# Kernel optimization log

Hardware: AMD Instinct MI355X
Metric: run time of the kernel (lower is better)

## Reference

```python
import jax, jax.numpy as jnp
import numpy as np

OUT_K = 7  # out_kernel


def setup_inputs() -> dict:
    key = jax.random.key(0)
    k = jax.random.split(key, 12)
    b, cin, h, w = 2, 256, 64, 64
    C, pd = 64, 4          # out_channels, pos_dim
    qc = C - pd            # channels produced by conv_q/k/v
    s = 0.05
    f32 = jnp.float32
    return {
        "x":    jax.random.normal(k[0], (b, cin, h, w), f32),
        "Wq":   jax.random.normal(k[1], (qc, cin), f32) * s,
        "bq":   jax.random.normal(k[2], (qc,), f32) * s,
        "Wk":   jax.random.normal(k[3], (qc, cin), f32) * s,
        "bk":   jax.random.normal(k[4], (qc,), f32) * s,
        "Wv":   jax.random.normal(k[5], (qc, cin), f32) * s,
        "bv":   jax.random.normal(k[6], (qc,), f32) * s,
        "Wp":   jax.random.normal(k[7], (pd, 2), f32) * s,
        "bp":   jax.random.normal(k[8], (pd,), f32) * s,
        "Wout": jax.random.normal(k[9], (C, C, OUT_K, OUT_K), f32) * s,
        "bout": jax.random.normal(k[10], (C,), f32) * s,
    }


def reference(x, Wq, bq, Wk, bk, Wv, bv, Wp, bp, Wout, bout):
    b, cin, h, w = x.shape
    C = Wout.shape[0]  # out_channels
    dt = x.dtype

    # positional encoding: hw_pose is (row_index, col_index) grids -> 1x1 conv to pos_dim chans
    rows = jnp.broadcast_to(jnp.arange(h, dtype=dt)[:, None], (h, w))
    cols = jnp.broadcast_to(jnp.arange(w, dtype=dt)[None, :], (h, w))
    grid = jnp.stack([rows, cols], axis=0)                      # (2,h,w)
    pos = jnp.einsum('oc,chw->ohw', Wp, grid) + bp[:, None, None]  # (pd,h,w)
    pos = jnp.broadcast_to(pos[None], (b,) + pos.shape)         # (b,pd,h,w)

    def conv1x1(W, bias):
        return jnp.einsum('bchw,oc->bohw', x, W) + bias[None, :, None, None]

    qs = jnp.concatenate([conv1x1(Wq, bq), pos], axis=1)        # (b,C,h,w)
    ks = jnp.concatenate([conv1x1(Wk, bk), pos], axis=1)
    vs = jnp.concatenate([conv1x1(Wv, bv), pos], axis=1)

    hw = h * w
    qsf = qs.transpose(0, 2, 3, 1).reshape(b, hw, C)            # (b,hw,C)
    ksf = ks.reshape(b, C, hw)                                  # (b,C,hw)
    vsf = vs.transpose(0, 2, 3, 1)                              # (b,h,w,C)

    qk = jnp.einsum('bnc,bcm->bnm', qsf, ksf) / jnp.sqrt(jnp.asarray(C, dt))
    diag = jnp.arange(hw)
    qk = qk.at[:, diag, diag].set(0.0)                          # zero diagonal BEFORE softmax
    attn = jax.nn.softmax(qk, axis=-1).reshape(b, h, w, h, w)

    # 7x7 clamped neighborhood gather (replaces the 49-iteration python loop)
    r = OUT_K // 2
    offs = jnp.arange(-r, r + 1)
    hi = jnp.clip(jnp.arange(h)[:, None] + offs[None, :], 0, h - 1)  # (h,7)
    wi = jnp.clip(jnp.arange(w)[:, None] + offs[None, :], 0, w - 1)  # (w,7)
    ii = jnp.arange(h)[:, None, None, None]
    jj = jnp.arange(w)[None, :, None, None]
    hk = hi[:, None, :, None]
    wk = wi[None, :, None, :]
    attn_loc = attn[:, ii, jj, hk, wk]                          # (b,h,w,7,7)
    v_loc = vsf[:, hk, wk, :]                                   # (b,h,w,7,7,C)

    qkv = attn_loc[..., None] * v_loc                           # (b,h,w,7,7,C)
    # con_out: kernel=7, stride=7 over a 7x7 patch == full contraction
    out = jnp.einsum('bhwklc,ockl->bhwo', qkv, Wout) + bout     # (b,h,w,C)
    out = jax.nn.relu(out)
    return out.transpose(0, 3, 1, 2)                            # (b,C,h,w)
```

## Files before the change

### kernel.cpp

```cpp
#include <hip/hip_runtime.h>
#include <math.h>

#define NTAP 49

typedef short bf16x8 __attribute__((ext_vector_type(8)));
typedef float f32x4  __attribute__((ext_vector_type(4)));

__device__ __forceinline__ float b2f(ushort u) {
    return __uint_as_float(((unsigned)u) << 16);
}
__device__ __forceinline__ ushort f2b(float f) {
    unsigned u = __float_as_uint(f);
    return (ushort)((u + 0x7FFFu + ((u >> 16) & 1u)) >> 16);
}
__device__ __forceinline__ int iclamp(int x) { return min(max(x, 0), 63); }

#define LOG2E 1.44269504f
#define S2    (0.125f * LOG2E)

#define WTB_OFF 0u
#define QH_OFF  598016u
#define KH_OFF  1646592u
#define VH_OFF  2695168u
#define LP_OFF  3743744u
#define MXQ_OFF 4005888u
#define MXK_OFF 4006912u

__device__ __forceinline__ float mh_reduce(const float* __restrict__ MXq,
                                           const float* __restrict__ MXk,
                                           int b, int t, float* sh) {
    if (t < 64) {
        float a = fmaxf(MXq[(b << 7) + t], MXq[(b << 7) + 64 + t]);
        float k = fmaxf(MXk[(b << 7) + t], MXk[(b << 7) + 64 + t]);
        #pragma unroll
        for (int off = 1; off < 64; off <<= 1) {
            a = fmaxf(a, __shfl_xor(a, off, 64));
            k = fmaxf(k, __shfl_xor(k, off, 64));
        }
        if (t == 0) *sh = 0.125f * sqrtf(a) * sqrtf(k) + 1.0f;
    }
    __syncthreads();
    return *sh;
}

__global__ __launch_bounds__(512, 2) void k_qkv(
    const float* __restrict__ x,
    const float* __restrict__ Wq, const float* __restrict__ Wk, const float* __restrict__ Wv,
    const float* __restrict__ bq, const float* __restrict__ bk, const float* __restrict__ bv,
    const float* __restrict__ Wp, const float* __restrict__ bp,
    ushort* __restrict__ QKV, float* __restrict__ MXq, float* __restrict__ MXk)
{
    __shared__ ushort Xh[32 * 256];
    __shared__ ushort Xl[32 * 256];
    __shared__ ushort Wshl[192 * 64];
    __shared__ float  sqL[64];
    int bid = blockIdx.x;
    int b   = bid >> 7;
    int n0  = (bid & 127) * 32;
    int t   = threadIdx.x;
    int w    = t >> 6;
    int L    = t & 63;
    int lrow = L & 15, lk = L >> 4;

    if (t < 64) sqL[t] = 0.f;
    {
        int p  = t & 31;
        int cg = t >> 5;
        #pragma unroll
        for (int it = 0; it < 2; ++it) {
            int cgi = cg + it * 16;
            float v[8];
            #pragma unroll
            for (int e = 0; e < 8; ++e)
                v[e] = x[((size_t)(b * 256 + cgi * 8 + e) << 12) + n0 + p];
            bf16x8 hi, lo;
            #pragma unroll
            for (int e = 0; e < 8; ++e) {
                ushort h = f2b(v[e]);
                hi[e] = (short)h;
                lo[e] = (short)f2b(v[e] - b2f(h));
            }
            int off = p * 256 + ((cgi * 8) ^ ((p & 7) * 8));
            *(bf16x8*)(Xh + off) = hi;
            *(bf16x8*)(Xl + off) = lo;
        }
    }

    int   s_och[3], s_g[3];
    bool  s_live[3];
    const float* s_src[3];
    #pragma unroll
    for (int s = 0; s < 3; ++s) {
        int g_idx = t + s * 512;
        int och = g_idx >> 3, g = g_idx & 7;
        int mat = och >> 6, o = och & 63;
        const float* Wm = (mat == 0) ? Wq : (mat == 1) ? Wk : Wv;
        s_och[s] = och; s_g[s] = g;
        s_live[s] = (o < 60);
        s_src[s] = Wm + o * 256 + (g & 3) * 8;
    }
    float4 wreg[3][2];

    #define ISSUE_W(c8) {                                                   \
        _Pragma("unroll")                                                   \
        for (int s = 0; s < 3; ++s) {                                       \
            if (s_live[s]) {                                                \
                const float* sp = s_src[s] + (c8) * 32;                     \
                wreg[s][0] = *(const float4*)(sp);                          \
                wreg[s][1] = *(const float4*)(sp + 4);                      \
            } else {                                                        \
                wreg[s][0] = make_float4(0.f,0.f,0.f,0.f);                  \
                wreg[s][1] = make_float4(0.f,0.f,0.f,0.f);                  \
            }                                                               \
        } }
    #define WRITE_W() {                                                     \
        _Pragma("unroll")                                                   \
        for (int s = 0; s < 3; ++s) {                                       \
            float vv[8] = {wreg[s][0].x, wreg[s][0].y, wreg[s][0].z,        \
                           wreg[s][0].w, wreg[s][1].x, wreg[s][1].y,        \
                           wreg[s][1].z, wreg[s][1].w};                     \
            bf16x8 val;                                                     \
            _Pragma("unroll")                                               \
            for (int e = 0; e < 8; ++e) {                                   \
                ushort h = f2b(vv[e]);                                      \
                val[e] = (s_g[s] < 4) ? (short)h                            \
                                      : (short)f2b(vv[e] - b2f(h));         \
            }                                                               \
            *(bf16x8*)((char*)Wshl + s_och[s] * 128 +                       \
                       ((s_g[s] * 16) ^ ((s_och[s] & 7) << 4))) = val;      \
        } }

    ISSUE_W(0);
    __syncthreads();
    WRITE_W();
    __syncthreads();

    int pxh = w >> 2;
    int ob  = (w & 3) * 48;
    int px  = pxh * 16 + lrow;

    f32x4 acc[3] = {{0,0,0,0},{0,0,0,0},{0,0,0,0}};

    for (int c8 = 0; c8 < 8; ++c8) {
        if (c8 + 1 < 8) ISSUE_W(c8 + 1);
        int cidx = (c8 * 4 + lk) * 8;
        int o0 = px * 256 + (cidx ^ ((px & 7) * 8));
        bf16x8 ah = *(const bf16x8*)(Xh + o0);
        bf16x8 al = *(const bf16x8*)(Xl + o0);
        #pragma unroll
        for (int c = 0; c < 3; ++c) {
            int och = ob + c * 16 + lrow;
            const char* wb = (const char*)Wshl + och * 128;
            int swz = (och & 7) << 4;
            bf16x8 bh = *(const bf16x8*)(wb + ((lk * 16) ^ swz));
            bf16x8 bl = *(const bf16x8*)(wb + (((4 + lk) * 16) ^ swz));
            acc[c] = __builtin_amdgcn_mfma_f32_16x16x32_bf16(al, bh, acc[c], 0, 0, 0);
            acc[c] = __builtin_amdgcn_mfma_f32_16x16x32_bf16(ah, bl, acc[c], 0, 0, 0);
            acc[c] = __builtin_amdgcn_mfma_f32_16x16x32_bf16(ah, bh, acc[c], 0, 0, 0);
        }
        __syncthreads();
        if (c8 + 1 < 8) WRITE_W();
        __syncthreads();
    }

    float s_q[4] = {0,0,0,0}, s_k[4] = {0,0,0,0};
    #pragma unroll
    for (int c = 0; c < 3; ++c) {
        int och = ob + c * 16 + lrow;
        int mat = och >> 6;
        int o   = och & 63;
        const float* bm = (mat == 0) ? bq : (mat == 1) ? bk : bv;
        ushort* Ob = QKV + (size_t)mat * 524288;
        if (o < 60) {
            float bias = bm[o];
            #pragma unroll
            for (int e = 0; e < 4; ++e) {
                int n = n0 + pxh * 16 + lk * 4 + e;
                float v = acc[c][e] + bias;
                Ob[((size_t)((b << 12) + n)) * 64 + o] = f2b(v);
                if (mat == 0) s_q[e] = fmaf(v, v, s_q[e]);
                else if (mat == 1) s_k[e] = fmaf(v, v, s_k[e]);
            }
        } else {
            int po = o - 60;
            float w0 = Wp[2 * po], w1 = Wp[2 * po + 1], b0 = bp[po];
            #pragma unroll
            for (int e = 0; e < 4; ++e) {
                int n = n0 + pxh * 16 + lk * 4 + e;
                float fi = (float)(n >> 6), fj = (float)(n & 63);
                float pv = fmaf(w0, fi, fmaf(w1, fj, b0));
                Ob[((size_t)((b << 12) + n)) * 64 + o] = f2b(pv);
                if (mat == 0) s_q[e] = fmaf(pv, pv, s_q[e]);
                else if (mat == 1) s_k[e] = fmaf(pv, pv, s_k[e]);
            }
        }
    }
    #pragma unroll
    for (int off = 1; off < 16; off <<= 1) {
        #pragma unroll
        for (int e = 0; e < 4; ++e) {
            s_q[e] += __shfl_xor(s_q[e], off, 64);
            s_k[e] += __shfl_xor(s_k[e], off, 64);
        }
    }
    if (lrow == 0) {
        #pragma unroll
        for (int e = 0; e < 4; ++e) {
            int pix = pxh * 16 + lk * 4 + e;
            atomicAdd(&sqL[pix],      s_q[e]);
            atomicAdd(&sqL[32 + pix], s_k[e]);
        }
    }
    __syncthreads();
    if (t < 32) {
        float q2 = sqL[t], k2 = sqL[32 + t];
        #pragma unroll
        for (int off = 1; off < 32; off <<= 1) {
            q2 = fmaxf(q2, __shfl_xor(q2, off, 64));
            k2 = fmaxf(k2, __shfl_xor(k2, off, 64));
        }
        if (t == 0) { MXq[bid] = q2; MXk[bid] = k2; }
    }
}

__global__ __launch_bounds__(512, 2) void k_stats(
    const float* __restrict__ Wout, ushort* __restrict__ Wtb,
    const ushort* __restrict__ QH, const ushort* __restrict__ KH,
    const float* __restrict__ MXq, const float* __restrict__ MXk,
    float* __restrict__ Lp)
{
    __shared__ ushort Ks[2][128 * 64];
    __shared__ float  mhs;
    int bid = blockIdx.x;
    int ks  = bid & 7;
    int r   = bid >> 3;
    int b   = r >> 5;
    int n0  = (r & 31) * 128;
    int ck0 = ks * 512;
    int t = threadIdx.x;

    {
        int widx = bid * 512 + t;
        if (widx < 64 * 64 * NTAP) {
            int o   = widx / (64 * NTAP);
            int rem = widx - o * (64 * NTAP);
            int c   = rem / NTAP;
            int kl  = rem - c * NTAP;
            Wtb[(o * NTAP + kl) * 64 + c] = f2b(Wout[widx]);
        }
    }
    float bse = -mh_reduce(MXq, MXk, b, t, &mhs) * LOG2E;

    int w = t >> 6, L = t & 63;
    int lrow = L & 15, lk = L >> 4;

    size_t qbase = ((size_t)((b << 12) + n0 + w * 16 + lrow)) * 64 + lk * 8;
    bf16x8 a0 = *(const bf16x8*)(QH + qbase);
    bf16x8 a1 = *(const bf16x8*)(QH + qbase + 32);

    #pragma unroll
    for (int gi = 0; gi < 2; ++gi) {
        int g = t + gi * 512;
        int u = g >> 3, c8 = g & 7;
        bf16x8 val = *(const bf16x8*)(KH + ((size_t)((b << 12) + ck0 + u)) * 64 + c8 * 8);
        *(bf16x8*)((char*)Ks[0] + u * 128 + ((c8 * 16) ^ ((u & 7) << 4))) = val;
    }

    float rs0 = 0.f, rs1 = 0.f, rs2 = 0.f, rs3 = 0.f;

    for (int c = 0; c < 4; ++c) {
        bf16x8 st0, st1;
        int u0 = t >> 3, c80 = t & 7;
        int u1 = (t + 512) >> 3, c81 = t & 7;
        bool pf = (c + 1) < 4;
        if (pf) {
            st0 = *(const bf16x8*)(KH + ((size_t)((b << 12) + ck0 + (c + 1) * 128 + u0)) * 64 + c80 * 8);
            st1 = *(const bf16x8*)(KH + ((size_t)((b << 12) + ck0 + (c + 1) * 128 + u1)) * 64 + c81 * 8);
        }
        __syncthreads();
        const char* kb = (const char*)Ks[c & 1];
        #pragma unroll
        for (int kg = 0; kg < 8; ++kg) {
            int u = kg * 16 + lrow;
            int swz = (u & 7) << 4;
            bf16x8 b0 = *(const bf16x8*)(kb + u * 128 + ((lk * 16) ^ swz));
            bf16x8 b1 = *(const bf16x8*)(kb + u * 128 + ((64 + lk * 16) ^ swz));
            f32x4 z = {0.f, 0.f, 0.f, 0.f};
            z = __builtin_amdgcn_mfma_f32_16x16x32_bf16(a0, b0, z, 0, 0, 0);
            z = __builtin_amdgcn_mfma_f32_16x16x32_bf16(a1, b1, z, 0, 0, 0);
            rs0 += exp2f(fmaf(z[0], S2, bse));
            rs1 += exp2f(fmaf(z[1], S2, bse));
            rs2 += exp2f(fmaf(z[2], S2, bse));
            rs3 += exp2f(fmaf(z[3], S2, bse));
        }
        if (pf) {
            char* kn = (char*)Ks[(c + 1) & 1];
            *(bf16x8*)(kn + u0 * 128 + ((c80 * 16) ^ ((u0 & 7) << 4))) = st0;
            *(bf16x8*)(kn + u1 * 128 + ((c81 * 16) ^ ((u1 & 7) << 4))) = st1;
        }
    }
    #pragma unroll
    for (int off = 1; off < 16; off <<= 1) {
        rs0 += __shfl_xor(rs0, off, 64);
        rs1 += __shfl_xor(rs1, off, 64);
        rs2 += __shfl_xor(rs2, off, 64);
        rs3 += __shfl_xor(rs3, off, 64);
    }
    if (lrow == 0) {
        float* dst = Lp + ((size_t)(ks * 2 + b) << 12) + n0 + w * 16 + lk * 4;
        dst[0] = rs0; dst[1] = rs1; dst[2] = rs2; dst[3] = rs3;
    }
}

__global__ __launch_bounds__(512, 2) void k_out(
    const ushort* __restrict__ QH, const ushort* __restrict__ KH,
    const ushort* __restrict__ VH, const ushort* __restrict__ Wtb,
    const float* __restrict__ Lp,
    const float* __restrict__ MXq, const float* __restrict__ MXk,
    const float* __restrict__ bout, float* __restrict__ out)
{
    __shared__ ushort Vs[7 * 40 * 64];
    __shared__ ushort Kh[7 * 40 * 64];
    __shared__ ushort Ws[7 * 64 * 64];
    __shared__ float  Al2[NTAP * 36];
    __shared__ float  Lrow[32];
    __shared__ float  LcS[32];
    __shared__ float  mhs;
    int bid = blockIdx.x;
    int b   = bid >> 7;
    int rem = bid & 127;
    int i   = rem >> 1;
    int j0  = (rem & 1) * 32;
    int n0  = (i << 6) + j0;
    int t   = threadIdx.x;
    int w    = t >> 6;
    int L    = t & 63;
    int lrow = L & 15, lk = L >> 4;

    float bse = -mh_reduce(MXq, MXk, b, t, &mhs) * LOG2E;
    float e0  = exp2f(bse);

    bf16x8 wreg[7];
    #define ISSUE_WS(kk) {                                                          \
        _Pragma("unroll")                                                           \
        for (int s = 0; s < 7; ++s) {                                               \
            int g = t + s * 512;                                                    \
            int c8 = g & 7, och = (g >> 3) & 63, ll = g >> 9;                       \
            wreg[s] = *(const bf16x8*)(Wtb + ((size_t)(och * NTAP + (kk) * 7 + ll)) * 64 + c8 * 8); \
        } }
    #define WRITE_WS() {                                                            \
        _Pragma("unroll")                                                           \
        for (int s = 0; s < 7; ++s) {                                               \
            int g = t + s * 512;                                                    \
            int c8 = g & 7, och = (g >> 3) & 63, ll = g >> 9;                       \
            *(bf16x8*)((char*)Ws + ll * 8192 + och * 128 +                          \
                       ((c8 * 16) ^ ((och & 7) << 4))) = wreg[s];                   \
        } }

    for (int g = t; g < 2 * 7 * 38 * 8; g += 512) {
        int which = g >= 7 * 38 * 8;
        int gg = which ? g - 7 * 38 * 8 : g;
        int kk = gg / 304;
        int r2 = gg - kk * 304;
        int u  = r2 >> 3, c8 = r2 & 7;
        int vr = iclamp(i + kk - 3);
        int vc = iclamp(j0 - 3 + u);
        const ushort* src = which ? KH : VH;
        ushort* dst = which ? Kh : Vs;
        bf16x8 val = *(const bf16x8*)(src + ((size_t)((b << 12) + (vr << 6) + vc)) * 64 + c8 * 8);
        *(bf16x8*)((char*)dst + kk * 5120 + u * 128 + ((c8 * 16) ^ ((u & 7) << 4))) = val;
    }
    ISSUE_WS(0);
    WRITE_WS();
    if (t < 32) {
        int n = n0 + t;
        float s = 0.f;
        #pragma unroll
        for (int ks = 0; ks < 8; ++ks)
            s += Lp[((size_t)(ks * 2 + b) << 12) + n];
        Lrow[t] = s;
    }
    __syncthreads();

    {
        int p = t >> 4, u = t & 15;
        int n = n0 + p;
        int pj = n & 63;
        const ushort* qr = QH + ((size_t)(b << 12) + n) * 64;
        bf16x8 qv[8];
        #pragma unroll
        for (int c8 = 0; c8 < 8; ++c8) qv[c8] = *(const bf16x8*)(qr + c8 * 8);

        int nt = (u == 0) ? 4 : 3;
        float d[4] = {0.f, 0.f, 0.f, 0.f};
        int srcs[4];
        const char* kbp[4];
        int swzs[4];
        #pragma unroll
        for (int m = 0; m < 4; ++m) {
            int tap = (m == 3) ? 48 : (u + 16 * m);
            int kk = tap / 7, ll = tap - kk * 7;
            srcs[m] = (iclamp(i + kk - 3) << 6) + iclamp(pj + ll - 3);
            int uu = p + ll;
            kbp[m]  = (const char*)Kh + kk * 5120 + uu * 128;
            swzs[m] = (uu & 7) << 4;
        }
        #pragma unroll
        for (int c8 = 0; c8 < 8; ++c8) {
            bf16x8 kv0 = *(const bf16x8*)(kbp[0] + ((c8 * 16) ^ swzs[0]));
            bf16x8 kv1 = *(const bf16x8*)(kbp[1] + ((c8 * 16) ^ swzs[1]));
            bf16x8 kv2 = *(const bf16x8*)(kbp[2] + ((c8 * 16) ^ swzs[2]));
            #pragma unroll
            for (int e = 0; e < 8; ++e) {
                float q = b2f((ushort)qv[c8][e]);
                d[0] = fmaf(q, b2f((ushort)kv0[e]), d[0]);
                d[1] = fmaf(q, b2f((ushort)kv1[e]), d[1]);
                d[2] = fmaf(q, b2f((ushort)kv2[e]), d[2]);
            }
        }
        if (nt == 4) {
            #pragma unroll
            for (int c8 = 0; c8 < 8; ++c8) {
                bf16x8 kv3 = *(const bf16x8*)(kbp[3] + ((c8 * 16) ^ swzs[3]));
                #pragma unroll
                for (int e = 0; e < 8; ++e)
                    d[3] = fmaf(b2f((ushort)qv[c8][e]), b2f((ushort)kv3[e]), d[3]);
            }
        }
        if (u == 8)
            LcS[p] = Lrow[p] - exp2f(fmaf(d[1], S2, bse)) + e0;
        __syncthreads();
        float rLc = 1.0f / LcS[p];
        for (int m = 0; m < nt; ++m) {
            int tap = (m == 3) ? 48 : (u + 16 * m);
            float A = (srcs[m] == n) ? (e0 * rLc)
                                     : (exp2f(fmaf(d[m], S2, bse)) * rLc);
            Al2[tap * 36 + p] = A;
        }
    }
    __syncthreads();

    int q16 = (w >> 2) << 4;
    int o16 = (w & 3) << 4;
    int oA  = o16 + lrow;
    int wswz = (oA & 7) << 4;
    f32x4 acc0 = {0.f, 0.f, 0.f, 0.f};

    for (int kk = 0; kk < 7; ++kk) {
        if (kk + 1 < 7) ISSUE_WS(kk + 1);
        const char* vrow = (const char*)Vs + kk * 5120;
        #pragma unroll
        for (int ll = 0; ll < 7; ++ll) {
            int kl = kk * 7 + ll;
            int u = q16 + lrow + ll;
            const char* vb = vrow + u * 128;
            int swz = (u & 7) << 4;
            bf16x8 v0 = *(const bf16x8*)(vb + ((lk * 16) ^ swz));
            bf16x8 v1 = *(const bf16x8*)(vb + ((64 + lk * 16) ^ swz));
            float4 av = *(const float4*)(&Al2[kl * 36 + q16 + lk * 4]);
            const char* wb = (const char*)Ws + ll * 8192 + oA * 128;
            bf16x8 b00 = *(const bf16x8*)(wb + ((lk * 16) ^ wswz));
            bf16x8 b01 = *(const bf16x8*)(wb + (((4 + lk) * 16) ^ wswz));
            f32x4 z = {0.f, 0.f, 0.f, 0.f};
            z = __builtin_amdgcn_mfma_f32_16x16x32_bf16(v0, b00, z, 0, 0, 0);
            z = __builtin_amdgcn_mfma_f32_16x16x32_bf16(v1, b01, z, 0, 0, 0);
            acc0[0] = fmaf(av.x, z[0], acc0[0]);
            acc0[1] = fmaf(av.y, z[1], acc0[1]);
            acc0[2] = fmaf(av.z, z[2], acc0[2]);
            acc0[3] = fmaf(av.w, z[3], acc0[3]);
        }
        __syncthreads();
        if (kk + 1 < 7) WRITE_WS();
        __syncthreads();
    }

    int o = oA;
    int nbase = n0 + q16 + lk * 4;
    float bb = bout[o];
    float4 v = make_float4(fmaxf(acc0[0] + bb, 0.f), fmaxf(acc0[1] + bb, 0.f),
                           fmaxf(acc0[2] + bb, 0.f), fmaxf(acc0[3] + bb, 0.f));
    *(float4*)(out + (((size_t)(b * 64 + o)) << 12) + nbase) = v;
}

extern "C" void kernel_launch(void* const* d_in, const int* in_sizes, int n_in,
                              void* d_out, int out_size, void* d_ws, size_t ws_size,
                              hipStream_t stream) {
    const float* x    = (const float*)d_in[0];
    const float* Wq   = (const float*)d_in[1];
    const float* bq   = (const float*)d_in[2];
    const float* Wk   = (const float*)d_in[3];
    const float* bk   = (const float*)d_in[4];
    const float* Wv   = (const float*)d_in[5];
    const float* bv   = (const float*)d_in[6];
    const float* Wp   = (const float*)d_in[7];
    const float* bp   = (const float*)d_in[8];
    const float* Wout = (const float*)d_in[9];
    const float* bout = (const float*)d_in[10];
    float* out = (float*)d_out;

    char* ws = (char*)d_ws;
    ushort* Wtb = (ushort*)(ws + WTB_OFF);
    ushort* QKV = (ushort*)(ws + QH_OFF);
    float*  Lp  = (float*)(ws + LP_OFF);
    float*  MXq = (float*)(ws + MXQ_OFF);
    float*  MXk = (float*)(ws + MXK_OFF);

    ushort* QH = QKV;
    ushort* KH = QKV + 524288;
    ushort* VH = QKV + 1048576;

    hipLaunchKernelGGL(k_qkv,   dim3(256), dim3(512), 0, stream,
                       x, Wq, Wk, Wv, bq, bk, bv, Wp, bp, QKV, MXq, MXk);
    hipLaunchKernelGGL(k_stats, dim3(512), dim3(512), 0, stream,
                       Wout, Wtb, QH, KH, MXq, MXk, Lp);
    hipLaunchKernelGGL(k_out,   dim3(256), dim3(512), 0, stream,
                       QH, KH, VH, Wtb, Lp, MXq, MXk, bout, out);
}
```

Baseline: 50.54 us.

## Split warps by tap in k_out and double rows per warp in row-sum kernel

The row-sum kernel now has each warp cover 32 query rows over half the key chunk, reusing each K fragment for two MFMA pairs. This doubles the number of partial-sum planes, and the LSE reader in k_out is widened to match. In k_out, warps are assigned one horizontal tap each (7 active of 8) and compute all 32x64 outputs, so W fragments are reused across two query tiles. A shared-memory cross-warp reduction then sums the per-warp results. Shared memory grows to about 136KB, which drops occupancy to one block per CU, and one warp sits idle in the main loop.

Result: slower. 54.09 us (+7.0%).

```diff
diff --git a/kernel.cpp b/kernel.cpp
--- a/kernel.cpp
+++ b/kernel.cpp
@@ -23,8 +23,8 @@
 #define KH_OFF  1646592u
 #define VH_OFF  2695168u
 #define LP_OFF  3743744u
-#define MXQ_OFF 4005888u
-#define MXK_OFF 4006912u
+#define MXQ_OFF 4268032u
+#define MXK_OFF 4269056u
 
 __device__ __forceinline__ float mh_reduce(const float* __restrict__ MXq,
                                            const float* __restrict__ MXk,
@@ -253,10 +253,14 @@
 
     int w = t >> 6, L = t & 63;
     int lrow = L & 15, lk = L >> 4;
-
-    size_t qbase = ((size_t)((b << 12) + n0 + w * 16 + lrow)) * 64 + lk * 8;
-    bf16x8 a0 = *(const bf16x8*)(QH + qbase);
-    bf16x8 a1 = *(const bf16x8*)(QH + qbase + 32);
+    int rg = w & 3, kh = w >> 2;
+    int rbase = n0 + rg * 32;
+
+    size_t qb = ((size_t)((b << 12) + rbase + lrow)) * 64 + lk * 8;
+    bf16x8 a0 = *(const bf16x8*)(QH + qb);
+    bf16x8 a1 = *(const bf16x8*)(QH + qb + 32);
+    bf16x8 a2 = *(const bf16x8*)(QH + qb + 1024);
+    bf16x8 a3 = *(const bf16x8*)(QH + qb + 1024 + 32);
 
     #pragma unroll
     for (int gi = 0; gi < 2; ++gi) {
@@ -266,7 +270,7 @@
         *(bf16x8*)((char*)Ks[0] + u * 128 + ((c8 * 16) ^ ((u & 7) << 4))) = val;
     }
 
-    float rs0 = 0.f, rs1 = 0.f, rs2 = 0.f, rs3 = 0.f;
+    float rs0=0,rs1=0,rs2=0,rs3=0,rs4=0,rs5=0,rs6=0,rs7=0;
 
     for (int c = 0; c < 4; ++c) {
         bf16x8 st0, st1;
@@ -280,18 +284,24 @@
         __syncthreads();
         const char* kb = (const char*)Ks[c & 1];
         #pragma unroll
-        for (int kg = 0; kg < 8; ++kg) {
-            int u = kg * 16 + lrow;
+        for (int kg = 0; kg < 4; ++kg) {
+            int u = kh * 64 + kg * 16 + lrow;
             int swz = (u & 7) << 4;
             bf16x8 b0 = *(const bf16x8*)(kb + u * 128 + ((lk * 16) ^ swz));
             bf16x8 b1 = *(const bf16x8*)(kb + u * 128 + ((64 + lk * 16) ^ swz));
-            f32x4 z = {0.f, 0.f, 0.f, 0.f};
-            z = __builtin_amdgcn_mfma_f32_16x16x32_bf16(a0, b0, z, 0, 0, 0);
-            z = __builtin_amdgcn_mfma_f32_16x16x32_bf16(a1, b1, z, 0, 0, 0);
-            rs0 += exp2f(fmaf(z[0], S2, bse));
-            rs1 += exp2f(fmaf(z[1], S2, bse));
-            rs2 += exp2f(fmaf(z[2], S2, bse));
-            rs3 += exp2f(fmaf(z[3], S2, bse));
+            f32x4 z0 = {0,0,0,0}, z1 = {0,0,0,0};
+            z0 = __builtin_amdgcn_mfma_f32_16x16x32_bf16(a0, b0, z0, 0, 0, 0);
+            z0 = __builtin_amdgcn_mfma_f32_16x16x32_bf16(a1, b1, z0, 0, 0, 0);
+            z1 = __builtin_amdgcn_mfma_f32_16x16x32_bf16(a2, b0, z1, 0, 0, 0);
+            z1 = __builtin_amdgcn_mfma_f32_16x16x32_bf16(a3, b1, z1, 0, 0, 0);
+            rs0 += exp2f(fmaf(z0[0], S2, bse));
+            rs1 += exp2f(fmaf(z0[1], S2, bse));
+            rs2 += exp2f(fmaf(z0[2], S2, bse));
+            rs3 += exp2f(fmaf(z0[3], S2, bse));
+            rs4 += exp2f(fmaf(z1[0], S2, bse));
+            rs5 += exp2f(fmaf(z1[1], S2, bse));
+            rs6 += exp2f(fmaf(z1[2], S2, bse));
+            rs7 += exp2f(fmaf(z1[3], S2, bse));
         }
         if (pf) {
             char* kn = (char*)Ks[(c + 1) & 1];
@@ -301,31 +311,41 @@
     }
     #pragma unroll
     for (int off = 1; off < 16; off <<= 1) {
-        rs0 += __shfl_xor(rs0, off, 64);
-        rs1 += __shfl_xor(rs1, off, 64);
-        rs2 += __shfl_xor(rs2, off, 64);
-        rs3 += __shfl_xor(rs3, off, 64);
+        rs0 += __shfl_xor(rs0, off, 64); rs1 += __shfl_xor(rs1, off, 64);
+        rs2 += __shfl_xor(rs2, off, 64); rs3 += __shfl_xor(rs3, off, 64);
+        rs4 += __shfl_xor(rs4, off, 64); rs5 += __shfl_xor(rs5, off, 64);
+        rs6 += __shfl_xor(rs6, off, 64); rs7 += __shfl_xor(rs7, off, 64);
     }
     if (lrow == 0) {
-        float* dst = Lp + ((size_t)(ks * 2 + b) << 12) + n0 + w * 16 + lk * 4;
+        int plane = ks * 2 + kh;
+        float* dst = Lp + ((size_t)(plane * 2 + b) << 12) + rbase + lk * 4;
         dst[0] = rs0; dst[1] = rs1; dst[2] = rs2; dst[3] = rs3;
-    }
-}
-
-__global__ __launch_bounds__(512, 2) void k_out(
+        dst[16] = rs4; dst[17] = rs5; dst[18] = rs6; dst[19] = rs7;
+    }
+}
+
+#define SM_VS   0
+#define SM_KH   35840
+#define SM_WS   71680
+#define SM_AL2  129024
+#define SM_LROW 136080
+#define SM_LCS  136208
+#define SM_MHS  136336
+__global__ __launch_bounds__(512, 1) void k_out(
     const ushort* __restrict__ QH, const ushort* __restrict__ KH,
     const ushort* __restrict__ VH, const ushort* __restrict__ Wtb,
     const float* __restrict__ Lp,
     const float* __restrict__ MXq, const float* __restrict__ MXk,
     const float* __restrict__ bout, float* __restrict__ out)
 {
-    __shared__ ushort Vs[7 * 40 * 64];
-    __shared__ ushort Kh[7 * 40 * 64];
-    __shared__ ushort Ws[7 * 64 * 64];
-    __shared__ float  Al2[NTAP * 36];
-    __shared__ float  Lrow[32];
-    __shared__ float  LcS[32];
-    __shared__ float  mhs;
+    __shared__ __align__(16) char smem[136448];
+    char*  Vsb  = smem + SM_VS;
+    char*  Khb  = smem + SM_KH;
+    char*  Wsb  = smem + SM_WS;
+    float* Al2  = (float*)(smem + SM_AL2);
+    float* Lrow = (float*)(smem + SM_LROW);
+    float* LcS  = (float*)(smem + SM_LCS);
+
     int bid = blockIdx.x;
     int b   = bid >> 7;
     int rem = bid & 127;
@@ -337,7 +357,7 @@
     int L    = t & 63;
     int lrow = L & 15, lk = L >> 4;
 
-    float bse = -mh_reduce(MXq, MXk, b, t, &mhs) * LOG2E;
+    float bse = -mh_reduce(MXq, MXk, b, t, (float*)(smem + SM_MHS)) * LOG2E;
     float e0  = exp2f(bse);
 
     bf16x8 wreg[7];
@@ -345,15 +365,15 @@
         _Pragma("unroll")                                                           \
         for (int s = 0; s < 7; ++s) {                                               \
             int g = t + s * 512;                                                    \
-            int c8 = g & 7, och = (g >> 3) & 63, ll = g >> 9;                       \
-            wreg[s] = *(const bf16x8*)(Wtb + ((size_t)(och * NTAP + (kk) * 7 + ll)) * 64 + c8 * 8); \
+            int c8 = g & 7, och = (g >> 3) & 63, ll2 = g >> 9;                      \
+            wreg[s] = *(const bf16x8*)(Wtb + ((size_t)(och * NTAP + (kk) * 7 + ll2)) * 64 + c8 * 8); \
         } }
     #define WRITE_WS() {                                                            \
         _Pragma("unroll")                                                           \
         for (int s = 0; s < 7; ++s) {                                               \
             int g = t + s * 512;                                                    \
-            int c8 = g & 7, och = (g >> 3) & 63, ll = g >> 9;                       \
-            *(bf16x8*)((char*)Ws + ll * 8192 + och * 128 +                          \
+            int c8 = g & 7, och = (g >> 3) & 63, ll2 = g >> 9;                      \
+            *(bf16x8*)(Wsb + ll2 * 8192 + och * 128 +                               \
                        ((c8 * 16) ^ ((och & 7) << 4))) = wreg[s];                   \
         } }
 
@@ -366,9 +386,9 @@
         int vr = iclamp(i + kk - 3);
         int vc = iclamp(j0 - 3 + u);
         const ushort* src = which ? KH : VH;
-        ushort* dst = which ? Kh : Vs;
+        char* dst = which ? Khb : Vsb;
         bf16x8 val = *(const bf16x8*)(src + ((size_t)((b << 12) + (vr << 6) + vc)) * 64 + c8 * 8);
-        *(bf16x8*)((char*)dst + kk * 5120 + u * 128 + ((c8 * 16) ^ ((u & 7) << 4))) = val;
+        *(bf16x8*)(dst + kk * 5120 + u * 128 + ((c8 * 16) ^ ((u & 7) << 4))) = val;
     }
     ISSUE_WS(0);
     WRITE_WS();
@@ -376,8 +396,8 @@
         int n = n0 + t;
         float s = 0.f;
         #pragma unroll
-        for (int ks = 0; ks < 8; ++ks)
-            s += Lp[((size_t)(ks * 2 + b) << 12) + n];
+        for (int p = 0; p < 16; ++p)
+            s += Lp[((size_t)(p * 2 + b) << 12) + n];
         Lrow[t] = s;
     }
     __syncthreads();
@@ -402,7 +422,7 @@
             int kk = tap / 7, ll = tap - kk * 7;
             srcs[m] = (iclamp(i + kk - 3) << 6) + iclamp(pj + ll - 3);
             int uu = p + ll;
-            kbp[m]  = (const char*)Kh + kk * 5120 + uu * 128;
+            kbp[m]  = Khb + kk * 5120 + uu * 128;
             swzs[m] = (uu & 7) << 4;
         }
         #pragma unroll
@@ -440,46 +460,73 @@
     }
     __syncthreads();
 
-    int q16 = (w >> 2) << 4;
-    int o16 = (w & 3) << 4;
-    int oA  = o16 + lrow;
-    int wswz = (oA & 7) << 4;
-    f32x4 acc0 = {0.f, 0.f, 0.f, 0.f};
+    int ll = w;
+    bool active = (w < 7);
+    f32x4 acc[2][4] = {{{0,0,0,0},{0,0,0,0},{0,0,0,0},{0,0,0,0}},
+                       {{0,0,0,0},{0,0,0,0},{0,0,0,0},{0,0,0,0}}};
 
     for (int kk = 0; kk < 7; ++kk) {
         if (kk + 1 < 7) ISSUE_WS(kk + 1);
-        const char* vrow = (const char*)Vs + kk * 5120;
-        #pragma unroll
-        for (int ll = 0; ll < 7; ++ll) {
+        if (active) {
             int kl = kk * 7 + ll;
-            int u = q16 + lrow + ll;
-            const char* vb = vrow + u * 128;
-            int swz = (u & 7) << 4;
-            bf16x8 v0 = *(const bf16x8*)(vb + ((lk * 16) ^ swz));
-            bf16x8 v1 = *(const bf16x8*)(vb + ((64 + lk * 16) ^ swz));
-            float4 av = *(const float4*)(&Al2[kl * 36 + q16 + lk * 4]);
-            const char* wb = (const char*)Ws + ll * 8192 + oA * 128;
-            bf16x8 b00 = *(const bf16x8*)(wb + ((lk * 16) ^ wswz));
-            bf16x8 b01 = *(const bf16x8*)(wb + (((4 + lk) * 16) ^ wswz));
-            f32x4 z = {0.f, 0.f, 0.f, 0.f};
-            z = __builtin_amdgcn_mfma_f32_16x16x32_bf16(v0, b00, z, 0, 0, 0);
-            z = __builtin_amdgcn_mfma_f32_16x16x32_bf16(v1, b01, z, 0, 0, 0);
-            acc0[0] = fmaf(av.x, z[0], acc0[0]);
-            acc0[1] = fmaf(av.y, z[1], acc0[1]);
-            acc0[2] = fmaf(av.z, z[2], acc0[2]);
-            acc0[3] = fmaf(av.w, z[3], acc0[3]);
+            const char* vrow = Vsb + kk * 5120;
+            bf16x8 va[2][2];
+            float4 av[2];
+            #pragma unroll
+            for (int qt = 0; qt < 2; ++qt) {
+                int u = qt * 16 + lrow + ll;
+                const char* vb = vrow + u * 128;
+                int swz = (u & 7) << 4;
+                va[qt][0] = *(const bf16x8*)(vb + ((lk * 16) ^ swz));
+                va[qt][1] = *(const bf16x8*)(vb + ((64 + lk * 16) ^ swz));
+                av[qt] = *(const float4*)(Al2 + kl * 36 + qt * 16 + lk * 4);
+            }
+            #pragma unroll
+            for (int ot = 0; ot < 4; ++ot) {
+                int oA = ot * 16 + lrow;
+                const char* wb = Wsb + ll * 8192 + oA * 128;
+                int wswz = (oA & 7) << 4;
+                bf16x8 b00 = *(const bf16x8*)(wb + ((lk * 16) ^ wswz));
+                bf16x8 b01 = *(const bf16x8*)(wb + (((4 + lk) * 16) ^ wswz));
+                #pragma unroll
+                for (int qt = 0; qt < 2; ++qt) {
+                    f32x4 z = {0.f, 0.f, 0.f, 0.f};
+                    z = __builtin_amdgcn_mfma_f32_16x16x32_bf16(va[qt][0], b00, z, 0, 0, 0);
+                    z = __builtin_amdgcn_mfma_f32_16x16x32_bf16(va[qt][1], b01, z, 0, 0, 0);
+                    acc[qt][ot][0] = fmaf(av[qt].x, z[0], acc[qt][ot][0]);
+                    acc[qt][ot][1] = fmaf(av[qt].y, z[1], acc[qt][ot][1]);
+                    acc[qt][ot][2] = fmaf(av[qt].z, z[2], acc[qt][ot][2]);
+                    acc[qt][ot][3] = fmaf(av[qt].w, z[3], acc[qt][ot][3]);
+                }
+            }
         }
         __syncthreads();
         if (kk + 1 < 7) WRITE_WS();
         __syncthreads();
     }
 
-    int o = oA;
-    int nbase = n0 + q16 + lk * 4;
-    float bb = bout[o];
-    float4 v = make_float4(fmaxf(acc0[0] + bb, 0.f), fmaxf(acc0[1] + bb, 0.f),
-                           fmaxf(acc0[2] + bb, 0.f), fmaxf(acc0[3] + bb, 0.f));
-    *(float4*)(out + (((size_t)(b * 64 + o)) << 12) + nbase) = v;
+    {
+        float* S = (float*)smem;
+        #pragma unroll
+        for (int qt = 0; qt < 2; ++qt)
+            #pragma unroll
+            for (int ot = 0; ot < 4; ++ot)
+                *(f32x4*)(S + w * 2048 + ((qt * 4 + ot) * 64 + L) * 4) = acc[qt][ot];
+        __syncthreads();
+        float4 s = make_float4(0.f, 0.f, 0.f, 0.f);
+        #pragma unroll
+        for (int ww = 0; ww < 8; ++ww) {
+            float4 p = *(const float4*)(S + ww * 2048 + t * 4);
+            s.x += p.x; s.y += p.y; s.z += p.z; s.w += p.w;
+        }
+        int qt = t >> 8, ot = (t >> 6) & 3, LL = t & 63;
+        int och = ot * 16 + (LL & 15);
+        int n   = n0 + qt * 16 + (LL >> 4) * 4;
+        float bb = bout[och];
+        float4 v = make_float4(fmaxf(s.x + bb, 0.f), fmaxf(s.y + bb, 0.f),
+                               fmaxf(s.z + bb, 0.f), fmaxf(s.w + bb, 0.f));
+        *(float4*)(out + (((size_t)(b * 64 + och)) << 12) + n) = v;
+    }
 }
 
 extern "C" void kernel_launch(void* const* d_in, const int* in_sizes, int n_in,
```
